# Performance work log

Hardware: AMD Instinct MI355X
Metric: run time of the kernel (lower is better)

Reference implementation:

```python
import jax, jax.numpy as jnp
import numpy as np


def setup_inputs() -> dict:
    key = jax.random.key(0)
    k1, k2 = jax.random.split(key)
    bs, slen, d = 32, 4096, 512
    # uniform (0,1): per-row means positive so log-det terms are finite
    m1 = jax.random.uniform(k1, (bs, slen, d), dtype=jnp.float32)
    m2 = jax.random.uniform(k2, (bs, slen, d), dtype=jnp.float32)
    return {"m1": m1, "m2": m2}


def reference(m1, m2):
    # Faithful to the torch module (note it swaps naming: row-variances act as
    # the mean vectors mu, row-means act as the diagonal covariance sigma).
    var1 = jnp.var(m1, axis=-1, ddof=1)   # (bs, len) -- torch .var is unbiased
    var2 = jnp.var(m2, axis=-1, ddof=1)
    var_avg = (var1 + var2) * 0.5
    mu1, mu2, mu_avg = var1, var2, var_avg
    sig1 = jnp.mean(m1, axis=-1)          # diagonal of sigma_1
    sig2 = jnp.mean(m2, axis=-1)
    sig_avg = (sig1 + sig2) * 0.5

    n = jnp.float32(m1.shape[1])          # len == n1 == n2

    # det(diag)/det(diag) then log == sum of log-ratios (stable, O(n) form of
    # the original det/inverse/matmul on diag_embed matrices)
    log_sig_avg = jnp.log(sig_avg)
    t1_1 = jnp.sum(log_sig_avg - jnp.log(sig1), axis=-1)
    t1_2 = jnp.sum(log_sig_avg - jnp.log(sig2), axis=-1)
    # trace(sigma_avg^{-1} @ sigma_i) for diagonal matrices
    inv_avg = 1.0 / sig_avg
    t2_1 = jnp.sum(sig1 * inv_avg, axis=-1)
    t2_2 = jnp.sum(sig2 * inv_avg, axis=-1)
    # (mu_avg - mu_i)^T sigma_avg^{-1} (mu_avg - mu_i)
    d1 = mu_avg - mu1
    d2 = mu_avg - mu2
    t3_1 = jnp.sum(d1 * d1 * inv_avg, axis=-1)
    t3_2 = jnp.sum(d2 * d2 * inv_avg, axis=-1)

    kl = 0.5 * (0.5 * (t1_1 - n + t2_1 + t3_1) + 0.5 * (t1_2 - n + t2_2 + t3_2))
    return jnp.mean(kl)  # reduction='mean'
```

## Files before the change

### kernel.cpp

```cpp
#include <hip/hip_runtime.h>

#define DCOLS 512
#define NROWS (32 * 4096)
#define GRID1 2048
#define BLOCK1 256
#define WAVES_PER_BLOCK (BLOCK1 / 64)

__global__ __launch_bounds__(BLOCK1) void kld_rows_kernel(
    const float* __restrict__ m1, const float* __restrict__ m2,
    float* __restrict__ partial) {
  const int lane = threadIdx.x & 63;
  const int wave = threadIdx.x >> 6;
  const int gwave = blockIdx.x * WAVES_PER_BLOCK + wave;
  const int nwaves = gridDim.x * WAVES_PER_BLOCK;

  float acc = 0.0f;

  for (int row = gwave; row < NROWS; row += nwaves) {
    const float4* r1 = (const float4*)(m1 + (size_t)row * DCOLS);
    const float4* r2 = (const float4*)(m2 + (size_t)row * DCOLS);
    float4 a0 = r1[lane];
    float4 a1 = r1[lane + 64];
    float4 b0 = r2[lane];
    float4 b1 = r2[lane + 64];

    float s1 = (a0.x + a0.y) + (a0.z + a0.w) + (a1.x + a1.y) + (a1.z + a1.w);
    float s2 = (b0.x + b0.y) + (b0.z + b0.w) + (b1.x + b1.y) + (b1.z + b1.w);
    float q1 = 0.0f, q2 = 0.0f;
    q1 = fmaf(a0.x, a0.x, q1); q1 = fmaf(a0.y, a0.y, q1);
    q1 = fmaf(a0.z, a0.z, q1); q1 = fmaf(a0.w, a0.w, q1);
    q1 = fmaf(a1.x, a1.x, q1); q1 = fmaf(a1.y, a1.y, q1);
    q1 = fmaf(a1.z, a1.z, q1); q1 = fmaf(a1.w, a1.w, q1);
    q2 = fmaf(b0.x, b0.x, q2); q2 = fmaf(b0.y, b0.y, q2);
    q2 = fmaf(b0.z, b0.z, q2); q2 = fmaf(b0.w, b0.w, q2);
    q2 = fmaf(b1.x, b1.x, q2); q2 = fmaf(b1.y, b1.y, q2);
    q2 = fmaf(b1.z, b1.z, q2); q2 = fmaf(b1.w, b1.w, q2);

    #pragma unroll
    for (int off = 32; off > 0; off >>= 1) {
      s1 += __shfl_xor(s1, off);
      q1 += __shfl_xor(q1, off);
      s2 += __shfl_xor(s2, off);
      q2 += __shfl_xor(q2, off);
    }

    const float inv_d = 1.0f / (float)DCOLS;
    const float inv_dm1 = 1.0f / (float)(DCOLS - 1);
    float sig1 = s1 * inv_d;
    float sig2 = s2 * inv_d;
    float var1 = (q1 - s1 * s1 * inv_d) * inv_dm1;
    float var2 = (q2 - s2 * s2 * inv_d) * inv_dm1;

    float sig_avg = 0.5f * (sig1 + sig2);
    float inv_avg = 1.0f / sig_avg;

    float t1 = __logf((sig_avg * sig_avg) / (sig1 * sig2));
    float t2c = (sig1 + sig2) * inv_avg - 2.0f;
    float dd = 0.5f * (var2 - var1);
    float t3 = 2.0f * dd * dd * inv_avg;

    acc += t1 + t2c + t3;
  }

  __shared__ float sacc[WAVES_PER_BLOCK];
  if (lane == 0) sacc[wave] = acc;
  __syncthreads();
  if (threadIdx.x == 0) {
    float s = 0.0f;
    #pragma unroll
    for (int w = 0; w < WAVES_PER_BLOCK; ++w) s += sacc[w];
    partial[blockIdx.x] = s;
  }
}

__global__ __launch_bounds__(256) void kld_final_kernel(
    const float* __restrict__ partial, int n, float* __restrict__ out) {
  float s = 0.0f;
  for (int i = threadIdx.x; i < n; i += blockDim.x) s += partial[i];
  #pragma unroll
  for (int off = 32; off > 0; off >>= 1) s += __shfl_xor(s, off);
  __shared__ float red[4];
  const int lane = threadIdx.x & 63;
  const int wave = threadIdx.x >> 6;
  if (lane == 0) red[wave] = s;
  __syncthreads();
  if (threadIdx.x == 0) {
    float t = (red[0] + red[1]) + (red[2] + red[3]);
    out[0] = t * (0.25f / 32.0f);
  }
}

extern "C" void kernel_launch(void* const* d_in, const int* in_sizes, int n_in,
                              void* d_out, int out_size, void* d_ws, size_t ws_size,
                              hipStream_t stream) {
  const float* m1 = (const float*)d_in[0];
  const float* m2 = (const float*)d_in[1];
  float* out = (float*)d_out;
  float* partial = (float*)d_ws;

  kld_rows_kernel<<<GRID1, BLOCK1, 0, stream>>>(m1, m2, partial);
  kld_final_kernel<<<1, 256, 0, stream>>>(partial, GRID1, out);
}
```

Baseline: 98.64 us.

## Process four rows per wave with 16-lane groups and deeper loads

Each wave now splits into four 16-lane groups, each reducing its own row, so every lane issues sixteen float4 loads per iteration instead of four. The row loop gets a compile-time trip count and is fully unrolled. The cross-lane reduction shortens to four shuffle steps, with two extra shuffles at the end to combine group accumulators. The goal is more bytes in flight per wave and less shuffle overhead, at the cost of higher register pressure and 256-byte rather than 1 KB contiguous segments per load instruction.

```diff
diff --git a/kernel.cpp b/kernel.cpp
--- a/kernel.cpp
+++ b/kernel.cpp
@@ -5,39 +5,49 @@
 #define GRID1 2048
 #define BLOCK1 256
 #define WAVES_PER_BLOCK (BLOCK1 / 64)
+#define ROWS_PER_ITER 4
+#define NWAVES (GRID1 * WAVES_PER_BLOCK)
+#define ITERS (NROWS / (NWAVES * ROWS_PER_ITER))
 
 __global__ __launch_bounds__(BLOCK1) void kld_rows_kernel(
     const float* __restrict__ m1, const float* __restrict__ m2,
     float* __restrict__ partial) {
   const int lane = threadIdx.x & 63;
+  const int sub  = lane & 15;
+  const int grp  = lane >> 4;
   const int wave = threadIdx.x >> 6;
   const int gwave = blockIdx.x * WAVES_PER_BLOCK + wave;
-  const int nwaves = gridDim.x * WAVES_PER_BLOCK;
 
   float acc = 0.0f;
 
-  for (int row = gwave; row < NROWS; row += nwaves) {
-    const float4* r1 = (const float4*)(m1 + (size_t)row * DCOLS);
-    const float4* r2 = (const float4*)(m2 + (size_t)row * DCOLS);
-    float4 a0 = r1[lane];
-    float4 a1 = r1[lane + 64];
-    float4 b0 = r2[lane];
-    float4 b1 = r2[lane + 64];
+  #pragma unroll
+  for (int i = 0; i < ITERS; ++i) {
+    const int row = (i * NWAVES + gwave) * ROWS_PER_ITER + grp;
+    const float4* __restrict__ r1 = (const float4*)(m1 + (size_t)row * DCOLS);
+    const float4* __restrict__ r2 = (const float4*)(m2 + (size_t)row * DCOLS);
 
-    float s1 = (a0.x + a0.y) + (a0.z + a0.w) + (a1.x + a1.y) + (a1.z + a1.w);
-    float s2 = (b0.x + b0.y) + (b0.z + b0.w) + (b1.x + b1.y) + (b1.z + b1.w);
-    float q1 = 0.0f, q2 = 0.0f;
-    q1 = fmaf(a0.x, a0.x, q1); q1 = fmaf(a0.y, a0.y, q1);
-    q1 = fmaf(a0.z, a0.z, q1); q1 = fmaf(a0.w, a0.w, q1);
-    q1 = fmaf(a1.x, a1.x, q1); q1 = fmaf(a1.y, a1.y, q1);
-    q1 = fmaf(a1.z, a1.z, q1); q1 = fmaf(a1.w, a1.w, q1);
-    q2 = fmaf(b0.x, b0.x, q2); q2 = fmaf(b0.y, b0.y, q2);
-    q2 = fmaf(b0.z, b0.z, q2); q2 = fmaf(b0.w, b0.w, q2);
-    q2 = fmaf(b1.x, b1.x, q2); q2 = fmaf(b1.y, b1.y, q2);
-    q2 = fmaf(b1.z, b1.z, q2); q2 = fmaf(b1.w, b1.w, q2);
+    float4 a[8], b[8];
+    #pragma unroll
+    for (int k = 0; k < 8; ++k) a[k] = r1[sub + k * 16];
+    #pragma unroll
+    for (int k = 0; k < 8; ++k) b[k] = r2[sub + k * 16];
+
+    float s1 = 0.0f, q1 = 0.0f, s2 = 0.0f, q2 = 0.0f;
+    #pragma unroll
+    for (int k = 0; k < 8; ++k) {
+      s1 += (a[k].x + a[k].y) + (a[k].z + a[k].w);
+      q1 = fmaf(a[k].x, a[k].x, q1); q1 = fmaf(a[k].y, a[k].y, q1);
+      q1 = fmaf(a[k].z, a[k].z, q1); q1 = fmaf(a[k].w, a[k].w, q1);
+    }
+    #pragma unroll
+    for (int k = 0; k < 8; ++k) {
+      s2 += (b[k].x + b[k].y) + (b[k].z + b[k].w);
+      q2 = fmaf(b[k].x, b[k].x, q2); q2 = fmaf(b[k].y, b[k].y, q2);
+      q2 = fmaf(b[k].z, b[k].z, q2); q2 = fmaf(b[k].w, b[k].w, q2);
+    }
 
     #pragma unroll
-    for (int off = 32; off > 0; off >>= 1) {
+    for (int off = 8; off > 0; off >>= 1) {
       s1 += __shfl_xor(s1, off);
       q1 += __shfl_xor(q1, off);
       s2 += __shfl_xor(s2, off);
@@ -61,6 +71,9 @@
 
     acc += t1 + t2c + t3;
   }
+
+  acc += __shfl_xor(acc, 16);
+  acc += __shfl_xor(acc, 32);
 
   __shared__ float sacc[WAVES_PER_BLOCK];
   if (lane == 0) sacc[wave] = acc;
```

After: 95.13 us. 3.6% less time.
